# Optimization experiments

Measured on AMD Instinct MI355X. Metric: run time of the kernel, lower is better.

## Reference

```python
import jax, jax.numpy as jnp
import numpy as np

PAD0, PAD1 = 2, 1  # Blur pad=(2,1), replicate_pad=False -> upfirdn2d pad
UPSAMPLE_FACTOR = 2


def _make_kernel():
    k = jnp.array([1.0, 3.0, 3.0, 1.0], dtype=jnp.float32)
    k2 = k[None, :] * k[:, None]
    k2 = k2 / jnp.sum(k2)
    return k2 * (UPSAMPLE_FACTOR ** 2)  # (4,4)


def setup_inputs() -> dict:
    key = jax.random.key(0)
    x = jax.random.normal(key, (8, 256, 256, 256), dtype=jnp.float32)
    kernel = _make_kernel()
    return {"x": x, "kernel": kernel}


def reference(x, kernel):
    # upfirdn2d with up=1, down=1, pad=(PAD0, PAD1): zero-pad then true
    # convolution with the FIR kernel (flip == cross-correlation kernel).
    N, C, H, W = x.shape
    kh, kw = kernel.shape
    xp = jnp.pad(x, ((0, 0), (0, 0), (PAD0, PAD1), (PAD0, PAD1)))
    k = jnp.flip(kernel)[None, None, :, :]  # (1,1,kh,kw), true convolution
    # depthwise: fold channels into batch, single-channel conv
    xr = xp.reshape(N * C, 1, H + PAD0 + PAD1, W + PAD0 + PAD1)
    out = jax.lax.conv_general_dilated(
        xr, k, window_strides=(1, 1), padding='VALID',
        dimension_numbers=('NCHW', 'OIHW', 'NCHW'))
    Ho = H + PAD0 + PAD1 - kh + 1
    Wo = W + PAD0 + PAD1 - kw + 1
    return out.reshape(N, C, Ho, Wo)
```

## Files before the change

kernel.cpp:

```cpp
#include <hip/hip_runtime.h>


constexpr int W = 256;
constexpr int H = 256;
constexpr float F0 = 0.25f;
constexpr float F1 = 0.75f;

typedef float f32x4 __attribute__((ext_vector_type(4)));

__device__ __forceinline__ f32x4 hfilt(const f32x4 v, const int lane) {
    float xl2 = __shfl_up(v.z, 1);
    float xl1 = __shfl_up(v.w, 1);
    float xr  = __shfl_down(v.x, 1);
    if (lane == 0)  { xl2 = 0.0f; xl1 = 0.0f; }
    if (lane == 63) { xr = 0.0f; }
    f32x4 h;
    h.x = F0 * xl2 + F1 * xl1 + F1 * v.x + F0 * v.y;
    h.y = F0 * xl1 + F1 * v.x + F1 * v.y + F0 * v.z;
    h.z = F0 * v.x + F1 * v.y + F1 * v.z + F0 * v.w;
    h.w = F0 * v.y + F1 * v.z + F1 * v.w + F0 * xr;
    return h;
}

__device__ __forceinline__ f32x4 vfilt(const f32x4 A, const f32x4 B,
                                       const f32x4 C, const f32x4 D) {
    f32x4 o;
    o.x = F0 * (A.x + D.x) + F1 * (B.x + C.x);
    o.y = F0 * (A.y + D.y) + F1 * (B.y + C.y);
    o.z = F0 * (A.z + D.z) + F1 * (B.z + C.z);
    o.w = F0 * (A.w + D.w) + F1 * (B.w + C.w);
    return o;
}

__global__ __launch_bounds__(256) void blur_kernel(const float* __restrict__ x,
                                                   float* __restrict__ out) {
    const int wave  = threadIdx.x >> 6;
    const int lane  = threadIdx.x & 63;
    const int plane = blockIdx.x * 4 + wave;
    const float* xp = x + (size_t)plane * (H * W);
    float*       op = out + (size_t)plane * (H * W);
    const int col = lane * 4;

    auto loadrow = [&](int i) -> f32x4 {
        if ((unsigned)i >= (unsigned)H) return f32x4{0.f, 0.f, 0.f, 0.f};
        return __builtin_nontemporal_load(
            reinterpret_cast<const f32x4*>(xp + i * W + col));
    };
    auto storerow = [&](int i, const f32x4 o) {
        __builtin_nontemporal_store(o, reinterpret_cast<f32x4*>(op + i * W + col));
    };

    f32x4 A = hfilt(loadrow(-2), lane);
    f32x4 B = hfilt(loadrow(-1), lane);
    f32x4 C = hfilt(loadrow(0), lane);

    f32x4 a0 = loadrow(1), a1 = loadrow(2), a2 = loadrow(3), a3 = loadrow(4);
    f32x4 b0 = loadrow(5), b1 = loadrow(6), b2 = loadrow(7), b3 = loadrow(8);

#pragma unroll 2
    for (int g = 0; g < 32; ++g) {
        const int base = 8 * g;
        const bool refill = (g < 31);

        f32x4 D0 = hfilt(a0, lane), D1 = hfilt(a1, lane),
              D2 = hfilt(a2, lane), D3 = hfilt(a3, lane);
        f32x4 o0 = vfilt(A,  B,  C,  D0);
        f32x4 o1 = vfilt(B,  C,  D0, D1);
        f32x4 o2 = vfilt(C,  D0, D1, D2);
        f32x4 o3 = vfilt(D0, D1, D2, D3);
        A = D1; B = D2; C = D3;
        if (refill) {
            a0 = loadrow(base + 9);  a1 = loadrow(base + 10);
            a2 = loadrow(base + 11); a3 = loadrow(base + 12);
        }
        storerow(base,     o0); storerow(base + 1, o1);
        storerow(base + 2, o2); storerow(base + 3, o3);

        f32x4 E0 = hfilt(b0, lane), E1 = hfilt(b1, lane),
              E2 = hfilt(b2, lane), E3 = hfilt(b3, lane);
        f32x4 p0 = vfilt(A,  B,  C,  E0);
        f32x4 p1 = vfilt(B,  C,  E0, E1);
        f32x4 p2 = vfilt(C,  E0, E1, E2);
        f32x4 p3 = vfilt(E0, E1, E2, E3);
        A = E1; B = E2; C = E3;
        if (refill) {
            b0 = loadrow(base + 13); b1 = loadrow(base + 14);
            b2 = loadrow(base + 15); b3 = loadrow(base + 16);
        }
        storerow(base + 4, p0); storerow(base + 5, p1);
        storerow(base + 6, p2); storerow(base + 7, p3);
    }
}

extern "C" void kernel_launch(void* const* d_in, const int* in_sizes, int n_in,
                              void* d_out, int out_size, void* d_ws, size_t ws_size,
                              hipStream_t stream) {
    const float* x = (const float*)d_in[0];
    float* o = (float*)d_out;
    const int planes = in_sizes[0] / (H * W);
    blur_kernel<<<planes / 4, 256, 0, stream>>>(x, o);
}
```

Measured before the change: 213.5 us.

## Split each plane into four 64-row strips, one per wave

Each block now handles one plane instead of four. Each of its four waves processes a 64-row strip, and odd waves walk their strip bottom-up. This gives four times as many blocks and a much shorter serial row loop per wave, which should improve occupancy and latency hiding on a bandwidth-bound kernel. The cost is re-reading halo rows at strip boundaries; those use normal cached loads so neighbouring waves can hit in cache. The fixed-trip loop is fully unrolled, which adds register pressure.

```diff
diff --git a/kernel.cpp b/kernel.cpp
--- a/kernel.cpp
+++ b/kernel.cpp
@@ -32,21 +32,22 @@
     return o;
 }
 
-__global__ __launch_bounds__(256) void blur_kernel(const float* __restrict__ x,
-                                                   float* __restrict__ out) {
-    const int wave  = threadIdx.x >> 6;
-    const int lane  = threadIdx.x & 63;
-    const int plane = blockIdx.x * 4 + wave;
-    const float* xp = x + (size_t)plane * (H * W);
-    float*       op = out + (size_t)plane * (H * W);
-    const int col = lane * 4;
-
-    auto loadrow = [&](int i) -> f32x4 {
+template <bool DOWN>
+__device__ __forceinline__ void do_strip(const float* __restrict__ xp,
+                                         float* __restrict__ op,
+                                         const int r0, const int lane,
+                                         const int col) {
+    auto loadrow = [&](int k) -> f32x4 {
+        const int off = DOWN ? k : 62 - k;
+        const int i = r0 + off;
         if ((unsigned)i >= (unsigned)H) return f32x4{0.f, 0.f, 0.f, 0.f};
-        return __builtin_nontemporal_load(
-            reinterpret_cast<const f32x4*>(xp + i * W + col));
+        const f32x4* p = reinterpret_cast<const f32x4*>(xp + i * W + col);
+        if (off <= 0 || off >= 62)
+            return *p;
+        return __builtin_nontemporal_load(p);
     };
-    auto storerow = [&](int i, const f32x4 o) {
+    auto storerow = [&](int k, const f32x4 o) {
+        const int i = r0 + (DOWN ? k : 63 - k);
         __builtin_nontemporal_store(o, reinterpret_cast<f32x4*>(op + i * W + col));
     };
 
@@ -57,10 +58,9 @@
     f32x4 a0 = loadrow(1), a1 = loadrow(2), a2 = loadrow(3), a3 = loadrow(4);
     f32x4 b0 = loadrow(5), b1 = loadrow(6), b2 = loadrow(7), b3 = loadrow(8);
 
-#pragma unroll 2
-    for (int g = 0; g < 32; ++g) {
+#pragma unroll
+    for (int g = 0; g < 8; ++g) {
         const int base = 8 * g;
-        const bool refill = (g < 31);
 
         f32x4 D0 = hfilt(a0, lane), D1 = hfilt(a1, lane),
               D2 = hfilt(a2, lane), D3 = hfilt(a3, lane);
@@ -69,7 +69,7 @@
         f32x4 o2 = vfilt(C,  D0, D1, D2);
         f32x4 o3 = vfilt(D0, D1, D2, D3);
         A = D1; B = D2; C = D3;
-        if (refill) {
+        if (g < 7) {
             a0 = loadrow(base + 9);  a1 = loadrow(base + 10);
             a2 = loadrow(base + 11); a3 = loadrow(base + 12);
         }
@@ -83,7 +83,7 @@
         f32x4 p2 = vfilt(C,  E0, E1, E2);
         f32x4 p3 = vfilt(E0, E1, E2, E3);
         A = E1; B = E2; C = E3;
-        if (refill) {
+        if (g < 7) {
             b0 = loadrow(base + 13); b1 = loadrow(base + 14);
             b2 = loadrow(base + 15); b3 = loadrow(base + 16);
         }
@@ -92,11 +92,27 @@
     }
 }
 
+__global__ __launch_bounds__(256) void blur_kernel(const float* __restrict__ x,
+                                                   float* __restrict__ out) {
+    const int plane = blockIdx.x;
+    const int wave  = threadIdx.x >> 6;
+    const int lane  = threadIdx.x & 63;
+    const float* xp = x + (size_t)plane * (H * W);
+    float*       op = out + (size_t)plane * (H * W);
+    const int r0  = wave * 64;
+    const int col = lane * 4;
+
+    if (wave & 1)
+        do_strip<false>(xp, op, r0, lane, col);
+    else
+        do_strip<true>(xp, op, r0, lane, col);
+}
+
 extern "C" void kernel_launch(void* const* d_in, const int* in_sizes, int n_in,
                               void* d_out, int out_size, void* d_ws, size_t ws_size,
                               hipStream_t stream) {
     const float* x = (const float*)d_in[0];
     float* o = (float*)d_out;
     const int planes = in_sizes[0] / (H * W);
-    blur_kernel<<<planes / 4, 256, 0, stream>>>(x, o);
+    blur_kernel<<<planes, 256, 0, stream>>>(x, o);
 }
```

Result: no change. 214.0 us (+0.3%).
